# Kernel optimization log

Measured on AMD Instinct MI355X. Metric: run time of the kernel, lower is better.

The kernel has to match this reference:

```python
import jax, jax.numpy as jnp
import numpy as np

N, M, D = 4096, 50000, 512


def setup_inputs() -> dict:
    key = jax.random.key(0)
    k1, k2, k3, k4, k5 = jax.random.split(key, 5)
    return {
        "X_trans": jax.random.normal(k1, (N, D), dtype=jnp.float32),
        "Y_tgt": jax.random.normal(k2, (N, D), dtype=jnp.float32),
        "Z_src": jax.random.normal(k3, (M, D), dtype=jnp.float32),
        "Z_tgt": jax.random.normal(k4, (M, D), dtype=jnp.float32),
        "back_emb": jax.random.normal(k5, (N, D), dtype=jnp.float32),
        "knn": 10,
    }


def _l2norm(x):
    # row-wise L2 normalize, matching x / x.norm(2,1,keepdim=True)
    return x / jnp.linalg.norm(x, axis=1, keepdims=True)


def _getknn(sc, k):
    # torch: topk(10) values gathered then sliced to first k, summed / k
    vals = jax.lax.top_k(sc, 10)[0]  # [rows, 10], sorted descending
    return vals[:, :k].sum() / k


def reference(X_trans, Y_tgt, Z_src, Z_tgt, back_emb, knn):
    src_emb = _l2norm(X_trans)
    tgt_emb = _l2norm(Y_tgt)
    zs = _l2norm(Z_src)
    zt = _l2norm(Z_tgt)
    bk = _l2norm(back_emb)
    f = 2.0 * jnp.sum(src_emb * tgt_emb)
    fk0 = _getknn(src_emb @ zt.T, knn)   # [N, M] scores src->tgt vocab
    fk1 = _getknn(bk @ zs.T, knn)        # [N, M] scores back->src vocab
    f = f - fk0 - fk1
    return -f / X_trans.shape[0]
```

## Files before the change

### kernel.cpp

```cpp
#include <hip/hip_runtime.h>
#include <hip/hip_bf16.h>
#include <stdint.h>

#define N_ROWS 4096
#define DIM 512
#define M_COLS 50000
#define GTOT (M_COLS/16)
#define SPLITS 8
#define TOPK 10

typedef __attribute__((ext_vector_type(8))) short bf16x8;
typedef __attribute__((ext_vector_type(4))) float f32x4;
typedef __attribute__((address_space(1))) const uint32_t gu32;
typedef __attribute__((address_space(3))) uint32_t lu32;

__device__ __forceinline__ float waveSum(float v){
  #pragma unroll
  for (int off=32; off>0; off>>=1) v += __shfl_xor(v, off, 64);
  return v;
}

__device__ __forceinline__ unsigned short f2bf(float x){
  __hip_bfloat16 h = __float2bfloat16(x);
  return *reinterpret_cast<unsigned short*>(&h);
}

__global__ __launch_bounds__(128) void norm_bf16_kernel(const float* __restrict__ in,
                                                        unsigned short* __restrict__ out){
  const int row = blockIdx.x;
  const int t = threadIdx.x;
  const float4 v = *reinterpret_cast<const float4*>(in + (size_t)row*DIM + t*4);
  float ss = v.x*v.x + v.y*v.y + v.z*v.z + v.w*v.w;
  ss = waveSum(ss);
  __shared__ float sred[2];
  if ((t & 63) == 0) sred[t>>6] = ss;
  __syncthreads();
  const float r = rsqrtf(sred[0] + sred[1]);
  ushort4 o;
  o.x = f2bf(v.x*r); o.y = f2bf(v.y*r); o.z = f2bf(v.z*r); o.w = f2bf(v.w*r);
  *reinterpret_cast<ushort4*>(out + (size_t)row*DIM + t*4) = o;
}

__global__ __launch_bounds__(128) void dotS_kernel(const float* __restrict__ X, const float* __restrict__ Y,
                                                   unsigned short* __restrict__ srcb, float* __restrict__ S_acc){
  const int row = blockIdx.x;
  const int t = threadIdx.x;
  const float4 x = *reinterpret_cast<const float4*>(X + (size_t)row*DIM + t*4);
  const float4 y = *reinterpret_cast<const float4*>(Y + (size_t)row*DIM + t*4);
  float ssx = x.x*x.x+x.y*x.y+x.z*x.z+x.w*x.w;
  float ssy = y.x*y.x+y.y*y.y+y.z*y.z+y.w*y.w;
  float sxy = x.x*y.x+x.y*y.y+x.z*y.z+x.w*y.w;
  ssx = waveSum(ssx); ssy = waveSum(ssy); sxy = waveSum(sxy);
  __shared__ float r0[2], r1[2], r2[2];
  if ((t&63)==0){ r0[t>>6]=ssx; r1[t>>6]=ssy; r2[t>>6]=sxy; }
  __syncthreads();
  const float tx = r0[0]+r0[1], ty = r1[0]+r1[1], txy = r2[0]+r2[1];
  const float rx = rsqrtf(tx);
  ushort4 o; o.x=f2bf(x.x*rx); o.y=f2bf(x.y*rx); o.z=f2bf(x.z*rx); o.w=f2bf(x.w*rx);
  *reinterpret_cast<ushort4*>(srcb + (size_t)row*DIM + t*4) = o;
  if (t == 0) atomicAdd(S_acc, txy * rsqrtf(tx*ty));
}

__global__ __launch_bounds__(256) void mm_topk_kernel(const unsigned short* __restrict__ A,
                                                      const unsigned short* __restrict__ Z,
                                                      float* __restrict__ topk){
  __shared__ __align__(16) unsigned short tiles[2][16*DIM];
  const int l = threadIdx.x & 63;
  const int w = threadIdx.x >> 6;
  const int rb = blockIdx.x;
  const int sp = blockIdx.y;
  const int gps = (GTOT + SPLITS - 1)/SPLITS;
  const int g0 = sp*gps;
  const int g1 = min(GTOT, g0 + gps);

  bf16x8 a[16];
  {
    const unsigned short* ap = A + (size_t)(rb*64 + w*16 + (l&15))*DIM + ((l>>4)*8);
    #pragma unroll
    for (int t=0; t<16; ++t) a[t] = *reinterpret_cast<const bf16x8*>(ap + 32*t);
  }

  float lst[4], thr[4];
  #pragma unroll
  for (int j=0;j<4;++j){ lst[j] = -__builtin_inff(); thr[j] = -__builtin_inff(); }

  auto stage = [&](int g, int b){
    const int c0 = g*16;
    #pragma unroll
    for (int q=0; q<4; ++q){
      const int i = w*4 + q;
      const unsigned short* src = Z + (size_t)(c0 + (l&15))*DIM + i*32 + (l>>4)*8;
      unsigned short* dst = &tiles[b][i*DIM];
      __builtin_amdgcn_global_load_lds((gu32*)src, (lu32*)dst, 16, 0, 0);
    }
  };

  stage(g0, 0);
  for (int g=g0; g<g1; ++g){
    const int buf = (g - g0) & 1;
    __syncthreads();
    if (g+1 < g1) stage(g+1, buf^1);
    f32x4 acc = {0.f,0.f,0.f,0.f};
    const unsigned short* tb = tiles[buf];
    #pragma unroll
    for (int t=0;t<16;++t){
      bf16x8 b = *reinterpret_cast<const bf16x8*>(tb + t*DIM + l*8);
      acc = __builtin_amdgcn_mfma_f32_16x16x32_bf16(a[t], b, acc, 0, 0, 0);
    }
    #pragma unroll
    for (int j=0;j<4;++j){
      bool myc = acc[j] > thr[j];
      unsigned long long m = __ballot(myc);
      while (m){
        const unsigned long long grp = (m >> (l & 48)) & 0xFFFFull;
        if (grp){
          const int src = (l & 48) + __builtin_ctzll(grp);
          const float v = __shfl(acc[j], src, 64);
          float nxt = __shfl(lst[j], (l==63)?63:(l+1), 64);
          if ((l & 15) >= 9) nxt = __builtin_inff();
          lst[j] = fminf(nxt, fmaxf(lst[j], v));
          thr[j] = __shfl(lst[j], l & 48, 64);
          if (l == src) myc = false;
        }
        m = __ballot(myc);
      }
    }
  }

  if ((l & 15) < TOPK){
    #pragma unroll
    for (int j=0;j<4;++j){
      const int row = rb*64 + w*16 + (l>>4)*4 + j;
      topk[((size_t)row*SPLITS + sp)*TOPK + (l & 15)] = lst[j];
    }
  }
}

__global__ __launch_bounds__(256) void merge_kernel(const float* __restrict__ tk, const int* __restrict__ knnp,
                                                    float* __restrict__ FK){
  const int n = blockIdx.x*256 + threadIdx.x;
  float ls[TOPK];
  #pragma unroll
  for (int i=0;i<TOPK;++i) ls[i] = -__builtin_inff();
  const float* p = tk + (size_t)n*(SPLITS*TOPK);
  for (int i=0;i<SPLITS*TOPK;++i){
    const float v = p[i];
    if (v > ls[0]){
      ls[0] = v;
      #pragma unroll
      for (int k=0;k<TOPK-1;++k){
        if (ls[k] > ls[k+1]){ float tmp=ls[k]; ls[k]=ls[k+1]; ls[k+1]=tmp; }
      }
    }
  }
  const int kk = min(max(knnp[0],1),TOPK);
  float s = 0.f;
  #pragma unroll
  for (int i=0;i<TOPK;++i) if (i < kk) s += ls[TOPK-1-i];
  s = waveSum(s);
  __shared__ float red[4];
  if ((threadIdx.x & 63)==0) red[threadIdx.x>>6] = s;
  __syncthreads();
  if (threadIdx.x==0) atomicAdd(FK, red[0]+red[1]+red[2]+red[3]);
}

__global__ void finalize_kernel(const float* __restrict__ S_acc, const float* __restrict__ FK,
                                const int* __restrict__ knnp, float* __restrict__ out){
  const float k = (float)max(knnp[0],1);
  out[0] = (FK[0]/k - 2.0f*S_acc[0]) / (float)N_ROWS;
}

extern "C" void kernel_launch(void* const* d_in, const int* in_sizes, int n_in,
                              void* d_out, int out_size, void* d_ws, size_t ws_size,
                              hipStream_t stream){
  const float* X  = (const float*)d_in[0];
  const float* Y  = (const float*)d_in[1];
  const float* Zs = (const float*)d_in[2];
  const float* Zt = (const float*)d_in[3];
  const float* Bk = (const float*)d_in[4];
  const int* knn  = (const int*)d_in[5];

  char* ws = (char*)d_ws;
  float* S_acc = (float*)ws;
  float* FK    = (float*)(ws + 4);
  float* topk0 = (float*)(ws + 64);
  float* topk1 = topk0 + (size_t)N_ROWS*SPLITS*TOPK;
  unsigned short* srcb = (unsigned short*)(ws + 64 + 2*(size_t)N_ROWS*SPLITS*TOPK*4);
  unsigned short* bkb  = srcb + (size_t)N_ROWS*DIM;
  unsigned short* Zb   = bkb  + (size_t)N_ROWS*DIM;

  hipMemsetAsync(d_ws, 0, 64, stream);
  dotS_kernel<<<N_ROWS, 128, 0, stream>>>(X, Y, srcb, S_acc);
  norm_bf16_kernel<<<N_ROWS, 128, 0, stream>>>(Bk, bkb);
  norm_bf16_kernel<<<M_COLS, 128, 0, stream>>>(Zt, Zb);
  mm_topk_kernel<<<dim3(N_ROWS/64, SPLITS), 256, 0, stream>>>(srcb, Zb, topk0);
  norm_bf16_kernel<<<M_COLS, 128, 0, stream>>>(Zs, Zb);
  mm_topk_kernel<<<dim3(N_ROWS/64, SPLITS), 256, 0, stream>>>(bkb, Zb, topk1);
  merge_kernel<<<(2*N_ROWS)/256, 256, 0, stream>>>(topk0, knn, FK);
  finalize_kernel<<<1, 1, 0, stream>>>(S_acc, FK, knn, (float*)d_out);
}
```

Baseline: 1.138 ms.

## Compute two row tiles per wave to reuse staged Z tiles, double splits

Each wave now holds A fragments for 32 rows and issues two MFMAs per loaded B fragment, so each staged Z tile in LDS and each global load serves twice as many rows. The grid row dimension is halved and SPLITS doubled to keep the number of blocks the same, with a launch-bounds hint for two blocks. This raises register use (two A fragment arrays and two top-k lists) and doubles the partial top-k lists the merge kernel scans.

```diff
diff --git a/kernel.cpp b/kernel.cpp
--- a/kernel.cpp
+++ b/kernel.cpp
@@ -6,7 +6,7 @@
 #define DIM 512
 #define M_COLS 50000
 #define GTOT (M_COLS/16)
-#define SPLITS 8
+#define SPLITS 16
 #define TOPK 10
 
 typedef __attribute__((ext_vector_type(8))) short bf16x8;
@@ -61,9 +61,9 @@
   if (t == 0) atomicAdd(S_acc, txy * rsqrtf(tx*ty));
 }
 
-__global__ __launch_bounds__(256) void mm_topk_kernel(const unsigned short* __restrict__ A,
-                                                      const unsigned short* __restrict__ Z,
-                                                      float* __restrict__ topk){
+__global__ __launch_bounds__(256, 2) void mm_topk_kernel(const unsigned short* __restrict__ A,
+                                                         const unsigned short* __restrict__ Z,
+                                                         float* __restrict__ topk){
   __shared__ __align__(16) unsigned short tiles[2][16*DIM];
   const int l = threadIdx.x & 63;
   const int w = threadIdx.x >> 6;
@@ -73,16 +73,21 @@
   const int g0 = sp*gps;
   const int g1 = min(GTOT, g0 + gps);
 
-  bf16x8 a[16];
+  bf16x8 a0[16], a1[16];
   {
-    const unsigned short* ap = A + (size_t)(rb*64 + w*16 + (l&15))*DIM + ((l>>4)*8);
-    #pragma unroll
-    for (int t=0; t<16; ++t) a[t] = *reinterpret_cast<const bf16x8*>(ap + 32*t);
-  }
-
-  float lst[4], thr[4];
-  #pragma unroll
-  for (int j=0;j<4;++j){ lst[j] = -__builtin_inff(); thr[j] = -__builtin_inff(); }
+    const unsigned short* ap = A + (size_t)(rb*128 + w*32 + (l&15))*DIM + ((l>>4)*8);
+    #pragma unroll
+    for (int t=0; t<16; ++t){
+      a0[t] = *reinterpret_cast<const bf16x8*>(ap + 32*t);
+      a1[t] = *reinterpret_cast<const bf16x8*>(ap + 16*DIM + 32*t);
+    }
+  }
+
+  float lst[2][4], thr[2][4];
+  #pragma unroll
+  for (int s=0;s<2;++s)
+    #pragma unroll
+    for (int j=0;j<4;++j){ lst[s][j] = -__builtin_inff(); thr[s][j] = -__builtin_inff(); }
 
   auto stage = [&](int g, int b){
     const int c0 = g*16;
@@ -95,44 +100,53 @@
     }
   };
 
-  stage(g0, 0);
-  for (int g=g0; g<g1; ++g){
-    const int buf = (g - g0) & 1;
-    __syncthreads();
-    if (g+1 < g1) stage(g+1, buf^1);
-    f32x4 acc = {0.f,0.f,0.f,0.f};
-    const unsigned short* tb = tiles[buf];
-    #pragma unroll
-    for (int t=0;t<16;++t){
-      bf16x8 b = *reinterpret_cast<const bf16x8*>(tb + t*DIM + l*8);
-      acc = __builtin_amdgcn_mfma_f32_16x16x32_bf16(a[t], b, acc, 0, 0, 0);
-    }
+  auto topk_update = [&](f32x4& acc, float* ls, float* th){
     #pragma unroll
     for (int j=0;j<4;++j){
-      bool myc = acc[j] > thr[j];
+      bool myc = acc[j] > th[j];
       unsigned long long m = __ballot(myc);
       while (m){
         const unsigned long long grp = (m >> (l & 48)) & 0xFFFFull;
         if (grp){
           const int src = (l & 48) + __builtin_ctzll(grp);
           const float v = __shfl(acc[j], src, 64);
-          float nxt = __shfl(lst[j], (l==63)?63:(l+1), 64);
+          float nxt = __shfl(ls[j], (l==63)?63:(l+1), 64);
           if ((l & 15) >= 9) nxt = __builtin_inff();
-          lst[j] = fminf(nxt, fmaxf(lst[j], v));
-          thr[j] = __shfl(lst[j], l & 48, 64);
+          ls[j] = fminf(nxt, fmaxf(ls[j], v));
+          th[j] = __shfl(ls[j], l & 48, 64);
           if (l == src) myc = false;
         }
         m = __ballot(myc);
       }
     }
+  };
+
+  stage(g0, 0);
+  for (int g=g0; g<g1; ++g){
+    const int buf = (g - g0) & 1;
+    __syncthreads();
+    if (g+1 < g1) stage(g+1, buf^1);
+    f32x4 acc0 = {0.f,0.f,0.f,0.f};
+    f32x4 acc1 = {0.f,0.f,0.f,0.f};
+    const unsigned short* tb = tiles[buf];
+    #pragma unroll
+    for (int t=0;t<16;++t){
+      bf16x8 b = *reinterpret_cast<const bf16x8*>(tb + t*DIM + l*8);
+      acc0 = __builtin_amdgcn_mfma_f32_16x16x32_bf16(a0[t], b, acc0, 0, 0, 0);
+      acc1 = __builtin_amdgcn_mfma_f32_16x16x32_bf16(a1[t], b, acc1, 0, 0, 0);
+    }
+    topk_update(acc0, lst[0], thr[0]);
+    topk_update(acc1, lst[1], thr[1]);
   }
 
   if ((l & 15) < TOPK){
     #pragma unroll
-    for (int j=0;j<4;++j){
-      const int row = rb*64 + w*16 + (l>>4)*4 + j;
-      topk[((size_t)row*SPLITS + sp)*TOPK + (l & 15)] = lst[j];
-    }
+    for (int s=0;s<2;++s)
+      #pragma unroll
+      for (int j=0;j<4;++j){
+        const int row = rb*128 + w*32 + s*16 + (l>>4)*4 + j;
+        topk[((size_t)row*SPLITS + sp)*TOPK + (l & 15)] = lst[s][j];
+      }
   }
 }
 
@@ -193,9 +207,9 @@
   dotS_kernel<<<N_ROWS, 128, 0, stream>>>(X, Y, srcb, S_acc);
   norm_bf16_kernel<<<N_ROWS, 128, 0, stream>>>(Bk, bkb);
   norm_bf16_kernel<<<M_COLS, 128, 0, stream>>>(Zt, Zb);
-  mm_topk_kernel<<<dim3(N_ROWS/64, SPLITS), 256, 0, stream>>>(srcb, Zb, topk0);
+  mm_topk_kernel<<<dim3(N_ROWS/128, SPLITS), 256, 0, stream>>>(srcb, Zb, topk0);
   norm_bf16_kernel<<<M_COLS, 128, 0, stream>>>(Zs, Zb);
-  mm_topk_kernel<<<dim3(N_ROWS/64, SPLITS), 256, 0, stream>>>(bkb, Zb, topk1);
+  mm_topk_kernel<<<dim3(N_ROWS/128, SPLITS), 256, 0, stream>>>(bkb, Zb, topk1);
   merge_kernel<<<(2*N_ROWS)/256, 256, 0, stream>>>(topk0, knn, FK);
   finalize_kernel<<<1, 1, 0, stream>>>(S_acc, FK, knn, (float*)d_out);
 }
```

Result: faster. 1.089 ms (-4.3%).
